# Kernel optimization log

Hardware: AMD Instinct MI355X
Metric: run time of the kernel (lower is better)

## Reference

```python
import jax, jax.numpy as jnp
import numpy as np

V, DH, E, KV = 30, 512, 256, 128  # vocab, decoder hidden, embed (=2*KV, tied), key/value dim
B, T, L = 256, 800, 300
SOS = 0


def _lstm_cell(x, h, c, w_ih, w_hh, b_ih, b_hh):
    g = x @ w_ih.T + b_ih + h @ w_hh.T + b_hh
    i, f, gg, o = jnp.split(g, 4, axis=-1)
    i, f, o = jax.nn.sigmoid(i), jax.nn.sigmoid(f), jax.nn.sigmoid(o)
    c2 = f * c + i * jnp.tanh(gg)
    return o * jnp.tanh(c2), c2


def setup_inputs() -> dict:
    key = jax.random.key(0)
    ks = jax.random.split(key, 12)
    emb = 0.1 * jax.random.normal(ks[0], (V, E), jnp.float32)
    emb = emb.at[0].set(0.0)  # padding_idx=0
    return {
        "key_enc": jax.random.normal(ks[1], (B, T, KV), jnp.float32),
        "value": jax.random.normal(ks[2], (B, T, KV), jnp.float32),
        "encoder_len": jax.random.randint(ks[3], (B,), 100, T + 1, jnp.int32),
        "y": jax.random.randint(ks[4], (B, L), 0, V, jnp.int64),
        "embedding": emb,  # also the tied character_prob weight (V, 2*KV)
        "w_ih1": 0.05 * jax.random.normal(ks[5], (4 * DH, E + KV), jnp.float32),
        "w_hh1": 0.05 * jax.random.normal(ks[6], (4 * DH, DH), jnp.float32),
        "b_ih1": jnp.zeros((4 * DH,), jnp.float32),
        "b_hh1": jnp.zeros((4 * DH,), jnp.float32),
        "w_ih2": 0.05 * jax.random.normal(ks[7], (4 * KV, DH), jnp.float32),
        "w_hh2": 0.05 * jax.random.normal(ks[8], (4 * KV, KV), jnp.float32),
        "b_ih2": jnp.zeros((4 * KV,), jnp.float32),
        "b_hh2": jnp.zeros((4 * KV,), jnp.float32),
        "out_bias": jnp.zeros((V,), jnp.float32),
    }


def reference(key_enc, value, encoder_len, y, embedding,
              w_ih1, w_hh1, b_ih1, b_hh1, w_ih2, w_hh2, b_ih2, b_hh2, out_bias):
    Bb, Tt, _ = key_enc.shape
    max_len = y.shape[1]
    valid = jnp.arange(Tt)[None, :] < encoder_len[:, None]  # (B, T)

    # teacher-forced embeddings: <sos> then y[:, :-1]
    sos = jnp.broadcast_to(embedding[SOS], (Bb, E))
    embeds = jnp.concatenate([sos[:, None, :], embedding[y[:, :-1]]], axis=1)  # (B, L, E)
    embeds = jnp.transpose(embeds, (1, 0, 2))  # (L, B, E)

    z1 = jnp.zeros((Bb, DH), key_enc.dtype)
    z2 = jnp.zeros((Bb, KV), key_enc.dtype)
    init = (z1, z1, z2, z2, value[:, 0, :])

    def step(carry, emb):
        h1, c1, h2, c2, ctx = carry
        x = jnp.concatenate([emb, ctx], axis=1)
        h1, c1 = _lstm_cell(x, h1, c1, w_ih1, w_hh1, b_ih1, b_hh1)
        h2, c2 = _lstm_cell(h1, h2, c2, w_ih2, w_hh2, b_ih2, b_hh2)
        q = h2  # (B, KV)
        energy = jnp.einsum('btk,bk->bt', key_enc, q)
        energy = jnp.where(valid, energy, -1e9)
        attn = jax.nn.softmax(energy, axis=-1)
        ctx = jnp.einsum('bt,btk->bk', attn, value)
        pred = jnp.concatenate([q, ctx], axis=1) @ embedding.T + out_bias  # tied weights
        return (h1, c1, h2, c2, ctx), (pred, attn[0])

    _, (preds, attn_plot) = jax.lax.scan(step, init, embeds)
    predictions = jnp.transpose(preds, (1, 0, 2))  # (B, L, V)
    return predictions, attn_plot  # attn_plot: (L, T)
```

## Files before the change

kernel.cpp:

```cpp
#include <hip/hip_runtime.h>
#include <cstddef>

#define NV   30
#define NDH  512
#define NE   256
#define NKV  128
#define NB   256
#define NT   800
#define NL   300
#define NKX  896

#define PRED_SIZE (NB*NL*NV)

typedef float v4f __attribute__((ext_vector_type(4)));
typedef float v2f __attribute__((ext_vector_type(2)));

#define OFF_XT  0
#define OFF_C1  229376
#define OFF_H2  (OFF_C1 + 131072)
#define OFF_C2  (OFF_H2 + 65536)
#define OFF_GP  (OFF_C2 + 32768)
#define OFF_BP  (OFF_GP + 2097152)

struct DecParams {
  const float* key; const float* val; const int* elen; const int* y;
  const float* emb;
  const float* wi1; const float* wh1; const float* bi1; const float* bh1;
  const float* wi2; const float* wh2; const float* bi2; const float* bh2;
  const float* ob;
  float* out; float* ws;
};

__device__ __forceinline__ float sigm(float x)  { return 1.0f/(1.0f + __expf(-x)); }
__device__ __forceinline__ float tanh_f(float x){ return 1.0f - 2.0f/(__expf(2.0f*x)+1.0f); }

__global__ void __launch_bounds__(256)
k_init(DecParams P)
{
  const int idx = blockIdx.x * 256 + threadIdx.x;
  float* ws = P.ws;
  if (idx < 229376) {
    const int row = idx >> 8, b = idx & 255;
    float v = 0.0f;
    if (row >= 256 && row < 384) v = P.val[(size_t)b*NT*NKV + (row-256)];
    ws[OFF_XT + idx] = v;
  } else {
    ws[idx] = 0.0f;
  }
}

__global__ void __launch_bounds__(256)
k_stepA(DecParams P)
{
  __shared__ float xs[32][68];
  __shared__ float wr[64][36];
  const int tid = threadIdx.x;
  const int bid = blockIdx.x;
  const int bt = bid & 3, jt = (bid >> 2) & 31, kt = bid >> 7;
  const int b0 = bt * 64, r0 = jt * 64;
  const int bq = tid & 15, rq = tid >> 4;

  const float* Xt = P.ws + OFF_XT;
  float* Gp = P.ws + OFF_GP;

  v4f acc[4];
#pragma unroll
  for (int i = 0; i < 4; ++i) acc[i] = (v4f)0.0f;

  const int kx_ld = tid >> 3, bx8 = (tid & 7) * 8;
  const int rw_ld = tid >> 2, kw8 = (tid & 3) * 8;

#pragma unroll 1
  for (int cc = 0; cc < 7; ++cc) {
    const int kg0 = kt * 224 + cc * 32;
    __syncthreads();
    {
      const v4f* src = (const v4f*)(Xt + (size_t)(kg0 + kx_ld) * 256 + b0 + bx8);
      v4f f0 = src[0], f1 = src[1];
      *(v4f*)&xs[kx_ld][bx8]     = f0;
      *(v4f*)&xs[kx_ld][bx8 + 4] = f1;
    }
    {
      const int row = r0 + rw_ld;
      const int kg = kg0 + kw8;
      const float* src = (kg < 384) ? (P.wi1 + (size_t)row*384 + kg)
                                    : (P.wh1 + (size_t)row*512 + (kg - 384));
      v4f f0 = ((const v4f*)src)[0], f1 = ((const v4f*)src)[1];
      *(v4f*)&wr[rw_ld][kw8]     = f0;
      *(v4f*)&wr[rw_ld][kw8 + 4] = f1;
    }
    __syncthreads();
#pragma unroll
    for (int q = 0; q < 8; ++q) {
      v4f x0 = *(const v4f*)&xs[q*4+0][bq*4];
      v4f x1 = *(const v4f*)&xs[q*4+1][bq*4];
      v4f x2 = *(const v4f*)&xs[q*4+2][bq*4];
      v4f x3 = *(const v4f*)&xs[q*4+3][bq*4];
#pragma unroll
      for (int ri = 0; ri < 4; ++ri) {
        v4f w = *(const v4f*)&wr[rq*4+ri][q*4];
        acc[ri] += w[0]*x0 + w[1]*x1 + w[2]*x2 + w[3]*x3;
      }
    }
  }
#pragma unroll
  for (int ri = 0; ri < 4; ++ri) {
    *(v4f*)&Gp[((size_t)kt*2048 + r0 + rq*4 + ri)*256 + b0 + bq*4] = acc[ri];
  }
}

__global__ void __launch_bounds__(256)
k_afin(DecParams P)
{
  const int j = blockIdx.x;
  const int b = threadIdx.x;
  const float* Gp = P.ws + OFF_GP;
  float* Xt = P.ws + OFF_XT;
  float* C1 = P.ws + OFF_C1;

  float s[4];
#pragma unroll
  for (int g = 0; g < 4; ++g) {
    const size_t base = ((size_t)g*512 + j)*256 + b;
    s[g] = Gp[base] + Gp[2048*256 + base] + Gp[2*2048*256 + base] + Gp[3*2048*256 + base]
         + P.bi1[g*512 + j] + P.bh1[g*512 + j];
  }
  const float ig = sigm(s[0]);
  const float fg = sigm(s[1]);
  const float gg = tanh_f(s[2]);
  const float og = sigm(s[3]);
  const float cn = fg * C1[(size_t)j*256 + b] + ig * gg;
  C1[(size_t)j*256 + b] = cn;
  Xt[(size_t)(384 + j)*256 + b] = og * tanh_f(cn);
}

__global__ void __launch_bounds__(256)
k_stepB(DecParams P, int t)
{
  __shared__ float xs2[32][36];
  __shared__ float wr2[32][36];
  const int tid = threadIdx.x;
  const int bid = blockIdx.x;
  const int bt = bid & 7, jt = (bid >> 3) & 15, kt = bid >> 7;
  const int b0 = bt * 32, r0 = jt * 32;
  const int bq = tid & 15, rq = tid >> 4;

  const float* Xt = P.ws + OFF_XT;
  const float* H2p = P.ws + OFF_H2 + (size_t)(t & 1) * 32768;
  float* Bp = P.ws + OFF_BP;

  v2f acc[2] = {(v2f)0.0f, (v2f)0.0f};

  const int kx_ld = tid >> 3, bx4 = (tid & 7) * 4;
  const int rw_ld = tid >> 3, kw4 = (tid & 7) * 4;

#pragma unroll 1
  for (int cc = 0; cc < 5; ++cc) {
    const int kg0 = kt * 160 + cc * 32;
    __syncthreads();
    {
      const int kg = kg0 + kx_ld;
      const float* src = (kg < 512) ? (Xt + (size_t)(384 + kg)*256 + b0 + bx4)
                                    : (H2p + (size_t)(kg - 512)*256 + b0 + bx4);
      *(v4f*)&xs2[kx_ld][bx4] = *(const v4f*)src;
    }
    {
      const int row = r0 + rw_ld;
      const int kg = kg0 + kw4;
      const float* src = (kg < 512) ? (P.wi2 + (size_t)row*512 + kg)
                                    : (P.wh2 + (size_t)row*128 + (kg - 512));
      *(v4f*)&wr2[rw_ld][kw4] = *(const v4f*)src;
    }
    __syncthreads();
#pragma unroll
    for (int p = 0; p < 16; ++p) {
      v2f x0 = *(const v2f*)&xs2[p*2+0][bq*2];
      v2f x1 = *(const v2f*)&xs2[p*2+1][bq*2];
#pragma unroll
      for (int ri = 0; ri < 2; ++ri) {
        v2f w = *(const v2f*)&wr2[rq*2+ri][p*2];
        acc[ri] += w[0]*x0 + w[1]*x1;
      }
    }
  }
#pragma unroll
  for (int bi = 0; bi < 2; ++bi) {
    v2f st; st[0] = acc[0][bi]; st[1] = acc[1][bi];
    *(v2f*)&Bp[((size_t)kt*256 + b0 + bq*2 + bi)*512 + r0 + rq*2] = st;
  }
}

__global__ void __launch_bounds__(512)
k_stepC(DecParams P, int t)
{
  __shared__ float e[NT];
  __shared__ float g2s[512];
  __shared__ float qc[256];
  __shared__ float red[16];
  __shared__ float ctxp[16][132];

  const int tid = threadIdx.x;
  const int b = blockIdx.x;
  const int len = P.elen[b];
  float* Xt = P.ws + OFF_XT;
  float* C2 = P.ws + OFF_C2;
  const float* Bp = P.ws + OFF_BP;
  float* H2n = P.ws + OFF_H2 + (size_t)((t + 1) & 1) * 32768;

  {
    const int r = tid;
    const size_t base = (size_t)b*512 + r;
    float s = Bp[base] + Bp[256*512 + base] + Bp[2*256*512 + base] + Bp[3*256*512 + base]
            + P.bi2[r] + P.bh2[r];
    g2s[r] = s;
  }
  __syncthreads();
  if (tid < 128) {
    const int j2 = tid;
    const float ig = sigm(g2s[j2]);
    const float fg = sigm(g2s[128 + j2]);
    const float gg = tanh_f(g2s[256 + j2]);
    const float og = sigm(g2s[384 + j2]);
    const float cn = fg * C2[(size_t)b*128 + j2] + ig * gg;
    C2[(size_t)b*128 + j2] = cn;
    const float h = og * tanh_f(cn);
    qc[j2] = h;
    H2n[(size_t)j2*256 + b] = h;
  }
  __syncthreads();

  const int lg = tid & 15, grp = tid >> 4;
  const v4f qa = *(const v4f*)&qc[lg*8];
  const v4f qb = *(const v4f*)&qc[lg*8 + 4];
  const v4f* kb = (const v4f*)(P.key + (size_t)b*NT*NKV);
#pragma unroll 1
  for (int s = 0; s < 13; ++s) {
    const int ta = s*64 + grp, tb = ta + 32;
    float pa = 0.0f, pb = 0.0f;
    if (ta < len) {
      v4f k0 = kb[(size_t)ta*32 + lg*2], k1 = kb[(size_t)ta*32 + lg*2 + 1];
      v4f d = k0*qa + k1*qb; pa = d[0]+d[1]+d[2]+d[3];
    }
    if (tb < len) {
      v4f k0 = kb[(size_t)tb*32 + lg*2], k1 = kb[(size_t)tb*32 + lg*2 + 1];
      v4f d = k0*qa + k1*qb; pb = d[0]+d[1]+d[2]+d[3];
    }
    pa += __shfl_xor(pa, 1); pb += __shfl_xor(pb, 1);
    pa += __shfl_xor(pa, 2); pb += __shfl_xor(pb, 2);
    pa += __shfl_xor(pa, 4); pb += __shfl_xor(pb, 4);
    pa += __shfl_xor(pa, 8); pb += __shfl_xor(pb, 8);
    if (lg == 0) {
      if (ta < len) e[ta] = pa;
      if (tb < len) e[tb] = pb;
    }
  }
  for (int tt = len + tid; tt < NT; tt += 512) e[tt] = -1e9f;
  __syncthreads();

  const int wid = tid >> 6;
  const float x0 = e[tid];
  const float x1 = (tid < NT - 512) ? e[512 + tid] : -3.0e38f;
  float m = fmaxf(x0, x1);
  m = fmaxf(m, __shfl_xor(m, 1));  m = fmaxf(m, __shfl_xor(m, 2));
  m = fmaxf(m, __shfl_xor(m, 4));  m = fmaxf(m, __shfl_xor(m, 8));
  m = fmaxf(m, __shfl_xor(m, 16)); m = fmaxf(m, __shfl_xor(m, 32));
  if ((tid & 63) == 0) red[wid] = m;
  __syncthreads();
  m = red[0];
#pragma unroll
  for (int i = 1; i < 8; ++i) m = fmaxf(m, red[i]);
  const float p0 = __expf(x0 - m);
  const float p1 = (tid < NT - 512) ? __expf(x1 - m) : 0.0f;
  float ss = p0 + p1;
  ss += __shfl_xor(ss, 1);  ss += __shfl_xor(ss, 2);  ss += __shfl_xor(ss, 4);
  ss += __shfl_xor(ss, 8);  ss += __shfl_xor(ss, 16); ss += __shfl_xor(ss, 32);
  if ((tid & 63) == 0) red[8 + wid] = ss;
  __syncthreads();
  float S = red[8];
#pragma unroll
  for (int i = 1; i < 8; ++i) S += red[8 + i];
  const float inv = 1.0f / S;
  e[tid] = p0 * inv;
  if (tid < NT - 512) e[512 + tid] = p1 * inv;
  if (b == 0) {
    P.out[PRED_SIZE + (size_t)t*NT + tid] = p0 * inv;
    if (tid < NT - 512) P.out[PRED_SIZE + (size_t)t*NT + 512 + tid] = p1 * inv;
  }
  __syncthreads();

  {
    const int kq = tid & 31, tq = tid >> 5;
    const v4f* vb = (const v4f*)(P.val + (size_t)b*NT*NKV);
    v4f a4 = (v4f)0.0f, a42 = (v4f)0.0f;
    int tt = tq;
    for (; tt + 16 < len; tt += 32) {
      a4  += e[tt]      * vb[(size_t)tt*32 + kq];
      a42 += e[tt + 16] * vb[(size_t)(tt + 16)*32 + kq];
    }
    if (tt < len) a4 += e[tt] * vb[(size_t)tt*32 + kq];
    a4 += a42;
    *(v4f*)&ctxp[tq][kq*4] = a4;
  }
  __syncthreads();
  if (tid < 128) {
    const int k = tid;
    float c = 0.0f;
#pragma unroll
    for (int r = 0; r < 16; ++r) c += ctxp[r][k];
    qc[128 + k] = c;
    Xt[(size_t)(256 + k)*256 + b] = c;
  }
  __syncthreads();

  {
    const int vv = tid >> 4, lg16 = tid & 15;
    if (vv < NV) {
      const v4f* er = (const v4f*)(P.emb + (size_t)vv*NE + lg16*16);
      const v4f* qr = (const v4f*)&qc[lg16*16];
      v4f s4 = er[0]*qr[0] + er[1]*qr[1] + er[2]*qr[2] + er[3]*qr[3];
      float p = s4[0] + s4[1] + s4[2] + s4[3];
      p += __shfl_xor(p, 1); p += __shfl_xor(p, 2);
      p += __shfl_xor(p, 4); p += __shfl_xor(p, 8);
      if (lg16 == 0) P.out[((size_t)b*NL + t)*NV + vv] = p + P.ob[vv];
    }
  }

  if (tid < 256) {
    const int tok = P.y[(size_t)b*NL + t];
    Xt[(size_t)tid*256 + b] = P.emb[(size_t)tok*NE + tid];
  }
}

extern "C" void kernel_launch(void* const* d_in, const int* in_sizes, int n_in,
                              void* d_out, int out_size, void* d_ws, size_t ws_size,
                              hipStream_t stream) {
  (void)in_sizes; (void)n_in; (void)out_size; (void)ws_size;
  DecParams P;
  P.key  = (const float*)d_in[0];
  P.val  = (const float*)d_in[1];
  P.elen = (const int*)d_in[2];
  P.y    = (const int*)d_in[3];
  P.emb  = (const float*)d_in[4];
  P.wi1  = (const float*)d_in[5];
  P.wh1  = (const float*)d_in[6];
  P.bi1  = (const float*)d_in[7];
  P.bh1  = (const float*)d_in[8];
  P.wi2  = (const float*)d_in[9];
  P.wh2  = (const float*)d_in[10];
  P.bi2  = (const float*)d_in[11];
  P.bh2  = (const float*)d_in[12];
  P.ob   = (const float*)d_in[13];
  P.out  = (float*)d_out;
  P.ws   = (float*)d_ws;

  hipLaunchKernelGGL(k_init, dim3(1792), dim3(256), 0, stream, P);
  for (int t = 0; t < NL; ++t) {
    hipLaunchKernelGGL(k_stepA, dim3(512), dim3(256), 0, stream, P);
    hipLaunchKernelGGL(k_afin,  dim3(512), dim3(256), 0, stream, P);
    hipLaunchKernelGGL(k_stepB, dim3(512), dim3(256), 0, stream, P, t);
    hipLaunchKernelGGL(k_stepC, dim3(NB),  dim3(512), 0, stream, P, t);
  }
}
```

Measured before the change: 17.86 ms.

## Use split-bf16 MFMA for LSTM layer-1 gate GEMM with pre-swizzled weights

Replaces the fp32 FMA tiled GEMM in stepA with bf16 MFMA 16x16x32 using a hi/lo split (three products) to keep near-fp32 accuracy. Weights are converted once to a fragment-ordered bf16 hi/lo layout. Activations are kept as batch-major bf16 hi/lo buffers written by afin and stepC. The K split drops from 4 to 2 partials, which halves the partial-sum reduction and the grid size. The cost is extra conversion work per step and lower parallelism in stepA.

```diff
diff --git a/kernel.cpp b/kernel.cpp
--- a/kernel.cpp
+++ b/kernel.cpp
@@ -14,13 +14,17 @@
 
 typedef float v4f __attribute__((ext_vector_type(4)));
 typedef float v2f __attribute__((ext_vector_type(2)));
+typedef short bf16x8 __attribute__((ext_vector_type(8)));
+typedef unsigned short ushort_t;
 
 #define OFF_XT  0
 #define OFF_C1  229376
-#define OFF_H2  (OFF_C1 + 131072)
-#define OFF_C2  (OFF_H2 + 65536)
-#define OFF_GP  (OFF_C2 + 32768)
-#define OFF_BP  (OFF_GP + 2097152)
+#define OFF_H2  360448
+#define OFF_C2  425984
+#define OFF_GP  458752
+#define OFF_BP  1507328
+#define OFF_XB  2031616
+#define OFF_WF  2293760
 
 struct DecParams {
   const float* key; const float* val; const int* elen; const int* y;
@@ -34,79 +38,124 @@
 __device__ __forceinline__ float sigm(float x)  { return 1.0f/(1.0f + __expf(-x)); }
 __device__ __forceinline__ float tanh_f(float x){ return 1.0f - 2.0f/(__expf(2.0f*x)+1.0f); }
 
+__device__ __forceinline__ ushort_t bf16_rne(float x){
+  union { float f; unsigned u; } v; v.f = x;
+  unsigned r = v.u + 0x7FFFu + ((v.u >> 16) & 1u);
+  return (ushort_t)(r >> 16);
+}
+__device__ __forceinline__ float bf16_to_f(ushort_t h){
+  union { float f; unsigned u; } v; v.u = ((unsigned)h) << 16;
+  return v.f;
+}
+
 __global__ void __launch_bounds__(256)
 k_init(DecParams P)
 {
   const int idx = blockIdx.x * 256 + threadIdx.x;
-  float* ws = P.ws;
-  if (idx < 229376) {
-    const int row = idx >> 8, b = idx & 255;
+  P.ws[idx] = 0.0f;
+}
+
+__global__ void __launch_bounds__(256)
+k_initX(DecParams P)
+{
+  const int b = blockIdx.x, tid = threadIdx.x;
+  ushort_t* xb = (ushort_t*)(P.ws + OFF_XB);
+  ushort_t* xbh = xb;
+  ushort_t* xbl = xb + 256*1024;
+#pragma unroll
+  for (int i = 0; i < 4; ++i) {
+    const int k = i*256 + tid;
     float v = 0.0f;
-    if (row >= 256 && row < 384) v = P.val[(size_t)b*NT*NKV + (row-256)];
-    ws[OFF_XT + idx] = v;
-  } else {
-    ws[idx] = 0.0f;
+    if (k >= 256 && k < 384) v = P.val[(size_t)b*NT*NKV + (k - 256)];
+    ushort_t hi = bf16_rne(v);
+    ushort_t lo = bf16_rne(v - bf16_to_f(hi));
+    xbh[(size_t)b*1024 + k] = hi;
+    xbl[(size_t)b*1024 + k] = lo;
+  }
+}
+
+__global__ void __launch_bounds__(256)
+k_initW(DecParams P)
+{
+  const int r = blockIdx.x;
+  const int tid = threadIdx.x;
+  ushort_t* wf = (ushort_t*)(P.ws + OFF_WF);
+  const int rt = r >> 4;
+#pragma unroll
+  for (int i = 0; i < 4; ++i) {
+    const int k = i*256 + tid;
+    if (k < NKX) {
+      const float w = (k < 384) ? P.wi1[(size_t)r*384 + k]
+                                : P.wh1[(size_t)r*512 + (k - 384)];
+      ushort_t hi = bf16_rne(w);
+      ushort_t lo = bf16_rne(w - bf16_to_f(hi));
+      const int kc = k >> 5;
+      const int lane = (r & 15) | (((k >> 3) & 3) << 4);
+      const int e = k & 7;
+      const size_t base = ((((size_t)rt)*28 + kc)*64 + lane)*8 + e;
+      wf[base] = hi;
+      wf[(size_t)128*28*64*8 + base] = lo;
+    }
   }
 }
 
 __global__ void __launch_bounds__(256)
 k_stepA(DecParams P)
 {
-  __shared__ float xs[32][68];
-  __shared__ float wr[64][36];
-  const int tid = threadIdx.x;
-  const int bid = blockIdx.x;
-  const int bt = bid & 3, jt = (bid >> 2) & 31, kt = bid >> 7;
-  const int b0 = bt * 64, r0 = jt * 64;
-  const int bq = tid & 15, rq = tid >> 4;
-
-  const float* Xt = P.ws + OFF_XT;
+  __shared__ ushort_t xs[2][64][72];
+  const int tid = threadIdx.x, bid = blockIdx.x;
+  const int mt = bid & 31, nt = (bid >> 5) & 3, kt = bid >> 7;
+  const int w = tid >> 6, lane = tid & 63;
+  const int rt16 = mt*4 + w;
+  const int b0 = nt * 64;
+
+  const ushort_t* Wf = (const ushort_t*)(P.ws + OFF_WF);
+  const ushort_t* Xb = (const ushort_t*)(P.ws + OFF_XB);
   float* Gp = P.ws + OFF_GP;
 
   v4f acc[4];
 #pragma unroll
   for (int i = 0; i < 4; ++i) acc[i] = (v4f)0.0f;
 
-  const int kx_ld = tid >> 3, bx8 = (tid & 7) * 8;
-  const int rw_ld = tid >> 2, kw8 = (tid & 3) * 8;
+  const int srow = tid >> 2, skq = (tid & 3) * 16;
+  const int lr = lane & 15, lk8 = (lane >> 4) * 8;
 
 #pragma unroll 1
-  for (int cc = 0; cc < 7; ++cc) {
-    const int kg0 = kt * 224 + cc * 32;
+  for (int p = 0; p < 7; ++p) {
+    const int kg = kt*448 + p*64;
     __syncthreads();
     {
-      const v4f* src = (const v4f*)(Xt + (size_t)(kg0 + kx_ld) * 256 + b0 + bx8);
-      v4f f0 = src[0], f1 = src[1];
-      *(v4f*)&xs[kx_ld][bx8]     = f0;
-      *(v4f*)&xs[kx_ld][bx8 + 4] = f1;
-    }
-    {
-      const int row = r0 + rw_ld;
-      const int kg = kg0 + kw8;
-      const float* src = (kg < 384) ? (P.wi1 + (size_t)row*384 + kg)
-                                    : (P.wh1 + (size_t)row*512 + (kg - 384));
-      v4f f0 = ((const v4f*)src)[0], f1 = ((const v4f*)src)[1];
-      *(v4f*)&wr[rw_ld][kw8]     = f0;
-      *(v4f*)&wr[rw_ld][kw8 + 4] = f1;
+      const ushort_t* s0 = Xb + (size_t)(b0 + srow)*1024 + kg + skq;
+      const ushort_t* s1 = s0 + (size_t)256*1024;
+      *(bf16x8*)&xs[0][srow][skq]     = *(const bf16x8*)(s0);
+      *(bf16x8*)&xs[0][srow][skq + 8] = *(const bf16x8*)(s0 + 8);
+      *(bf16x8*)&xs[1][srow][skq]     = *(const bf16x8*)(s1);
+      *(bf16x8*)&xs[1][srow][skq + 8] = *(const bf16x8*)(s1 + 8);
     }
     __syncthreads();
 #pragma unroll
-    for (int q = 0; q < 8; ++q) {
-      v4f x0 = *(const v4f*)&xs[q*4+0][bq*4];
-      v4f x1 = *(const v4f*)&xs[q*4+1][bq*4];
-      v4f x2 = *(const v4f*)&xs[q*4+2][bq*4];
-      v4f x3 = *(const v4f*)&xs[q*4+3][bq*4];
-#pragma unroll
-      for (int ri = 0; ri < 4; ++ri) {
-        v4f w = *(const v4f*)&wr[rq*4+ri][q*4];
-        acc[ri] += w[0]*x0 + w[1]*x1 + w[2]*x2 + w[3]*x3;
+    for (int kc2 = 0; kc2 < 2; ++kc2) {
+      const int kcg = (kg >> 5) + kc2;
+      bf16x8 ah = *(const bf16x8*)(Wf + ((((size_t)0*128 + rt16)*28 + kcg)*64 + lane)*8);
+      bf16x8 al = *(const bf16x8*)(Wf + ((((size_t)1*128 + rt16)*28 + kcg)*64 + lane)*8);
+      const int lk = kc2*32 + lk8;
+#pragma unroll
+      for (int ct = 0; ct < 4; ++ct) {
+        bf16x8 bh = *(const bf16x8*)&xs[0][ct*16 + lr][lk];
+        bf16x8 bl = *(const bf16x8*)&xs[1][ct*16 + lr][lk];
+        acc[ct] = __builtin_amdgcn_mfma_f32_16x16x32_bf16(ah, bh, acc[ct], 0, 0, 0);
+        acc[ct] = __builtin_amdgcn_mfma_f32_16x16x32_bf16(ah, bl, acc[ct], 0, 0, 0);
+        acc[ct] = __builtin_amdgcn_mfma_f32_16x16x32_bf16(al, bh, acc[ct], 0, 0, 0);
       }
     }
   }
-#pragma unroll
-  for (int ri = 0; ri < 4; ++ri) {
-    *(v4f*)&Gp[((size_t)kt*2048 + r0 + rq*4 + ri)*256 + b0 + bq*4] = acc[ri];
-  }
+  const int rg = (lane >> 4) * 4;
+  const int r0 = rt16 * 16;
+#pragma unroll
+  for (int ct = 0; ct < 4; ++ct)
+#pragma unroll
+    for (int j = 0; j < 4; ++j)
+      Gp[((size_t)kt*2048 + r0 + rg + j)*256 + b0 + ct*16 + lr] = acc[ct][j];
 }
 
 __global__ void __launch_bounds__(256)
@@ -117,12 +166,13 @@
   const float* Gp = P.ws + OFF_GP;
   float* Xt = P.ws + OFF_XT;
   float* C1 = P.ws + OFF_C1;
+  ushort_t* xb = (ushort_t*)(P.ws + OFF_XB);
 
   float s[4];
 #pragma unroll
   for (int g = 0; g < 4; ++g) {
     const size_t base = ((size_t)g*512 + j)*256 + b;
-    s[g] = Gp[base] + Gp[2048*256 + base] + Gp[2*2048*256 + base] + Gp[3*2048*256 + base]
+    s[g] = Gp[base] + Gp[(size_t)2048*256 + base]
          + P.bi1[g*512 + j] + P.bh1[g*512 + j];
   }
   const float ig = sigm(s[0]);
@@ -131,7 +181,12 @@
   const float og = sigm(s[3]);
   const float cn = fg * C1[(size_t)j*256 + b] + ig * gg;
   C1[(size_t)j*256 + b] = cn;
-  Xt[(size_t)(384 + j)*256 + b] = og * tanh_f(cn);
+  const float h = og * tanh_f(cn);
+  Xt[(size_t)(384 + j)*256 + b] = h;
+  ushort_t hi = bf16_rne(h);
+  ushort_t lo = bf16_rne(h - bf16_to_f(hi));
+  xb[(size_t)b*1024 + 384 + j] = hi;
+  xb[(size_t)256*1024 + (size_t)b*1024 + 384 + j] = lo;
 }
 
 __global__ void __launch_bounds__(256)
@@ -202,10 +257,11 @@
   const int tid = threadIdx.x;
   const int b = blockIdx.x;
   const int len = P.elen[b];
-  float* Xt = P.ws + OFF_XT;
   float* C2 = P.ws + OFF_C2;
   const float* Bp = P.ws + OFF_BP;
   float* H2n = P.ws + OFF_H2 + (size_t)((t + 1) & 1) * 32768;
+  ushort_t* xbh = (ushort_t*)(P.ws + OFF_XB);
+  ushort_t* xbl = xbh + (size_t)256*1024;
 
   {
     const int r = tid;
@@ -308,7 +364,10 @@
 #pragma unroll
     for (int r = 0; r < 16; ++r) c += ctxp[r][k];
     qc[128 + k] = c;
-    Xt[(size_t)(256 + k)*256 + b] = c;
+    ushort_t hi = bf16_rne(c);
+    ushort_t lo = bf16_rne(c - bf16_to_f(hi));
+    xbh[(size_t)b*1024 + 256 + k] = hi;
+    xbl[(size_t)b*1024 + 256 + k] = lo;
   }
   __syncthreads();
 
@@ -327,7 +386,11 @@
 
   if (tid < 256) {
     const int tok = P.y[(size_t)b*NL + t];
-    Xt[(size_t)tid*256 + b] = P.emb[(size_t)tok*NE + tid];
+    const float x = P.emb[(size_t)tok*NE + tid];
+    ushort_t hi = bf16_rne(x);
+    ushort_t lo = bf16_rne(x - bf16_to_f(hi));
+    xbh[(size_t)b*1024 + tid] = hi;
+    xbl[(size_t)b*1024 + tid] = lo;
   }
 }
 
@@ -353,9 +416,11 @@
   P.out  = (float*)d_out;
   P.ws   = (float*)d_ws;
 
-  hipLaunchKernelGGL(k_init, dim3(1792), dim3(256), 0, stream, P);
+  hipLaunchKernelGGL(k_init,  dim3(1792), dim3(256), 0, stream, P);
+  hipLaunchKernelGGL(k_initX, dim3(256),  dim3(256), 0, stream, P);
+  hipLaunchKernelGGL(k_initW, dim3(2048), dim3(256), 0, stream, P);
   for (int t = 0; t < NL; ++t) {
-    hipLaunchKernelGGL(k_stepA, dim3(512), dim3(256), 0, stream, P);
+    hipLaunchKernelGGL(k_stepA, dim3(256), dim3(256), 0, stream, P);
     hipLaunchKernelGGL(k_afin,  dim3(512), dim3(256), 0, stream, P);
     hipLaunchKernelGGL(k_stepB, dim3(512), dim3(256), 0, stream, P, t);
     hipLaunchKernelGGL(k_stepC, dim3(NB),  dim3(512), 0, stream, P, t);
```

Result: faster. 14.94 ms (-16.4%).
